# Kernel optimization log

Hardware: AMD Instinct MI355X
Metric: run time of the kernel (lower is better)

Reference implementation:

```python
import jax, jax.numpy as jnp
import numpy as np
import math

H_IMG, W_IMG = 800, 1216
STRIDES = [4, 8, 16, 32, 64]
SIZES = [32, 64, 128, 256, 512]
RATIOS = [0.5, 1.0, 2.0]
NUM_PER_LEVEL = [(-(-H_IMG // s)) * (-(-W_IMG // s)) * len(RATIOS) for s in STRIDES]
A_TOTAL = sum(NUM_PER_LEVEL)  # 728973
B = 4
PRE_NMS = 1000   # pre_nms_top_n['testing']
POST_NMS = 1000  # post_nms_top_n['testing']
NMS_TH = 0.7
MIN_SIZE = 1e-3
BBOX_XFORM_CLIP = math.log(1000.0 / 16)
NEG = -1e10
LEVELS_NP = np.repeat(np.arange(len(NUM_PER_LEVEL)), NUM_PER_LEVEL).astype(np.int32)


def _make_anchors():
    out = []
    for stride, size in zip(STRIDES, SIZES):
        fh, fw = -(-H_IMG // stride), -(-W_IMG // stride)
        r = np.sqrt(np.asarray(RATIOS, dtype=np.float64))
        ws, hs = size / r, size * r
        base = np.stack([-ws / 2, -hs / 2, ws / 2, hs / 2], axis=1)  # [3,4]
        sx = np.arange(fw, dtype=np.float64) * stride
        sy = np.arange(fh, dtype=np.float64) * stride
        gy, gx = np.meshgrid(sy, sx, indexing='ij')
        shifts = np.stack([gx.ravel(), gy.ravel(), gx.ravel(), gy.ravel()], axis=1)
        out.append((shifts[:, None, :] + base[None]).reshape(-1, 4))
    return np.concatenate(out, 0).astype(np.float32)


def setup_inputs() -> dict:
    key = jax.random.key(0)
    k1, k2 = jax.random.split(key)
    objectness = jax.random.normal(k1, (B, A_TOTAL), dtype=jnp.float32)
    deltas = jax.random.normal(k2, (B, A_TOTAL, 4), dtype=jnp.float32) * 0.2
    anchors = jnp.asarray(_make_anchors())
    return {'objectness': objectness, 'deltas': deltas, 'anchors': anchors}


def _decode(deltas, anchors):
    # BoxCoder.decode with weights (1,1,1,1)
    wa = anchors[:, 2] - anchors[:, 0]
    ha = anchors[:, 3] - anchors[:, 1]
    cxa = anchors[:, 0] + 0.5 * wa
    cya = anchors[:, 1] + 0.5 * ha
    dx, dy = deltas[..., 0], deltas[..., 1]
    dw = jnp.minimum(deltas[..., 2], BBOX_XFORM_CLIP)
    dh = jnp.minimum(deltas[..., 3], BBOX_XFORM_CLIP)
    cx = dx * wa + cxa
    cy = dy * ha + cya
    w = jnp.exp(dw) * wa
    h = jnp.exp(dh) * ha
    return jnp.stack([cx - 0.5 * w, cy - 0.5 * h, cx + 0.5 * w, cy + 0.5 * h], axis=-1)


def _topk_per_level(obj):
    # _get_top_n_idx: independent top-k within each anchor level, indices offset
    idxs, off = [], 0
    for n in NUM_PER_LEVEL:
        k = min(PRE_NMS, n)
        _, ti = jax.lax.top_k(obj[:, off:off + n], k)
        idxs.append(ti + off)
        off += n
    return jnp.concatenate(idxs, axis=1)


def _pairwise_iou(b):
    area = (b[:, 2] - b[:, 0]) * (b[:, 3] - b[:, 1])
    lt = jnp.maximum(b[:, None, :2], b[None, :, :2])
    rb = jnp.minimum(b[:, None, 2:], b[None, :, 2:])
    wh = jnp.clip(rb - lt, 0.0)
    inter = wh[..., 0] * wh[..., 1]
    return inter / (area[:, None] + area[None, :] - inter)


def _filter_image(boxes, scores, lvl):
    # clip_boxes_to_image
    x1 = jnp.clip(boxes[:, 0], 0.0, W_IMG)
    y1 = jnp.clip(boxes[:, 1], 0.0, H_IMG)
    x2 = jnp.clip(boxes[:, 2], 0.0, W_IMG)
    y2 = jnp.clip(boxes[:, 3], 0.0, H_IMG)
    boxes = jnp.stack([x1, y1, x2, y2], axis=1)
    # remove_small_boxes (as a validity mask; fixed shapes under jit)
    valid = ((x2 - x1) >= MIN_SIZE) & ((y2 - y1) >= MIN_SIZE)
    scores = jnp.where(valid, scores, NEG)
    N = boxes.shape[0]
    # batched_nms: offset boxes per level so levels never overlap
    sg_boxes = jax.lax.stop_gradient(boxes)
    offset = lvl.astype(boxes.dtype) * (sg_boxes.max() + 1.0)
    order = jnp.argsort(-jax.lax.stop_gradient(scores))
    iou = _pairwise_iou(sg_boxes[order] + offset[order][:, None])  # [N,N]
    idx = jnp.arange(N)
    def body(i, keep):
        sup = (iou[i] > NMS_TH) & keep[i] & (idx > i)
        return keep & ~sup
    keep = jax.lax.fori_loop(0, N, body, valid[order])
    # kept entries in score order, then truncate to POST_NMS (fixed shape)
    prio = jnp.where(keep, idx, N)
    sel = jnp.argsort(prio)[:POST_NMS]
    kept = keep[sel]
    src = order[sel]
    out_b = jnp.where(kept[:, None], boxes[src], 0.0)
    out_s = jnp.where(kept, scores[src], NEG)
    return out_b, out_s


def reference(objectness, deltas, anchors):
    proposals = _decode(deltas, anchors)                      # [B,A,4]
    top_idx = _topk_per_level(objectness)                     # [B,5000]
    obj_sel = jnp.take_along_axis(objectness, top_idx, axis=1)
    prop_sel = jnp.take_along_axis(proposals, top_idx[..., None], axis=1)
    lvl_sel = jnp.asarray(LEVELS_NP)[top_idx]
    boxes, scores = jax.vmap(_filter_image)(prop_sel, obj_sel, lvl_sel)
    return boxes, scores  # [B,POST_NMS,4], [B,POST_NMS]
```

## Files before the change

kernel.cpp:

```cpp
#include <hip/hip_runtime.h>
#include <stdint.h>

#pragma clang fp contract(off)

#define B_IMGS   4
#define NLVL     5
#define A_TOTAL  242991
#define NSEL     4741
#define NBUCK    8192
#define BSHIFT   19
#define CAND_CAP 2048
#define POST_NMS 1000
#define NBL      (B_IMGS * NLVL)
#define NMS_TH   0.7f
#define NEGV     (-1e10f)
#define W_IMGF   1216.0f
#define H_IMGF   800.0f
#define MIN_SZ   1e-3f
#define BBOX_CLIP 4.135166556742356f

__device__ __forceinline__ int lvl_k(int l) { return (l == 4) ? 741 : 1000; }

__device__ __forceinline__ unsigned flipf(float f) {
    unsigned u = __float_as_uint(f);
    return u ^ (unsigned)(((int)u >> 31) | 0x80000000);
}
__device__ __forceinline__ float unflipf(unsigned os) {
    unsigned u = (os & 0x80000000u) ? (os ^ 0x80000000u) : ~os;
    return __uint_as_float(u);
}

__device__ __forceinline__ void async_cp16(const void* g, void* l) {
    __builtin_amdgcn_global_load_lds(
        (const __attribute__((address_space(1))) unsigned*)g,
        (__attribute__((address_space(3))) unsigned*)l,
        16, 0, 0);
}

static constexpr size_t SZ_HIST    = (size_t)NBL * NBUCK * sizeof(unsigned);
static constexpr size_t OFF_CNT    = SZ_HIST;
static constexpr size_t OFF_BOXMAX = OFF_CNT + NBL * sizeof(unsigned);
static constexpr size_t ZERO_BYTES = OFF_BOXMAX + B_IMGS * sizeof(unsigned);
static constexpr size_t OFF_CAND   = (ZERO_BYTES + 15) & ~(size_t)15;
static constexpr size_t OFF_SEL    = OFF_CAND + (size_t)NBL * CAND_CAP * 8;
static constexpr size_t OFF_BOXR   = OFF_SEL + (size_t)B_IMGS * NSEL * 8;
static constexpr size_t OFF_SCR    = OFF_BOXR + (size_t)B_IMGS * NSEL * 16;
static constexpr size_t OFF_BOXL   = OFF_SCR + (size_t)B_IMGS * NSEL * 4;
static constexpr size_t OFF_VAL    = OFF_BOXL + (size_t)B_IMGS * NSEL * 16;
static constexpr size_t OFF_RMAP   = OFF_VAL + (size_t)B_IMGS * NSEL * 4;
static constexpr size_t OFF_KEEP   = OFF_RMAP + (size_t)B_IMGS * NSEL * 4;
static constexpr size_t OFF_MASK   = OFF_KEEP + (size_t)B_IMGS * NSEL * 4;
static constexpr size_t WS_NEED    = OFF_MASK + (size_t)NBL * 1024 * 16 * 8;

#define HBLK_PER_IMG 34
__global__ void k_hist(const float* __restrict__ obj, unsigned* __restrict__ hist) {
    __shared__ unsigned lh[NBUCK];
    const int tid = threadIdx.x;
    const int b = blockIdx.x / HBLK_PER_IMG;
    const int r = blockIdx.x - b * HBLK_PER_IMG;
    int l, sub, chunk, lstart, n;
    if (r < 24)      { l = 0; sub = r;      chunk = 7600; lstart = 0;      n = 182400; }
    else if (r < 30) { l = 1; sub = r - 24; chunk = 7600; lstart = 182400; n = 45600; }
    else if (r < 32) { l = 2; sub = r - 30; chunk = 5700; lstart = 228000; n = 11400; }
    else if (r == 32){ l = 3; sub = 0;      chunk = 2850; lstart = 239400; n = 2850; }
    else             { l = 4; sub = 0;      chunk = 741;  lstart = 242250; n = 741; }
    #pragma unroll
    for (int i = tid; i < NBUCK; i += 512) lh[i] = 0;
    __syncthreads();
    const int s0 = sub * chunk;
    const int cnt = min(chunk, n - s0);
    const float* src = obj + (size_t)b * A_TOTAL + lstart + s0;
    for (int i = tid; i < cnt; i += 512) {
        unsigned os = flipf(src[i]);
        atomicAdd(&lh[os >> BSHIFT], 1u);
    }
    __syncthreads();
    unsigned* gh = hist + (size_t)(b * NLVL + l) * NBUCK;
    for (int i = tid; i < NBUCK; i += 512) {
        unsigned v = lh[i];
        if (v) atomicAdd(&gh[i], v);
    }
}

#define CBLK_PER_IMG 65
__global__ void k_compact(const float* __restrict__ obj, const unsigned* __restrict__ hist,
                          unsigned* __restrict__ cnt, unsigned long long* __restrict__ cand) {
    __shared__ unsigned long long sbuf[CAND_CAP];
    __shared__ unsigned part[256];
    __shared__ unsigned wsum[4];
    __shared__ unsigned fcnt[4];
    __shared__ unsigned s_cum, s_thr, lcnt, gbase;
    const int tid = threadIdx.x;
    const int b = blockIdx.x / CBLK_PER_IMG;
    const int r = blockIdx.x - b * CBLK_PER_IMG;
    int l, sub, chunk, lstart, n;
    if (r < 48)      { l = 0; sub = r;      chunk = 3800; lstart = 0;      n = 182400; }
    else if (r < 60) { l = 1; sub = r - 48; chunk = 3800; lstart = 182400; n = 45600; }
    else if (r < 63) { l = 2; sub = r - 60; chunk = 3800; lstart = 228000; n = 11400; }
    else if (r == 63){ l = 3; sub = 0;      chunk = 2850; lstart = 239400; n = 2850; }
    else             { l = 4; sub = 0;      chunk = 741;  lstart = 242250; n = 741; }
    const int bl = b * NLVL + l;
    const int kl = lvl_k(l);
    const unsigned* h = hist + (size_t)bl * NBUCK;
    {
        unsigned s = 0;
        for (int i = 0; i < 32; ++i) s += h[tid * 32 + i];
        part[tid] = s;
    }
    if (tid == 0) { lcnt = 0; s_cum = 0; }
    __syncthreads();
    const int lane = tid & 63, wv = tid >> 6;
    unsigned x = part[255 - tid];
    #pragma unroll
    for (int d = 1; d < 64; d <<= 1) {
        unsigned up = __shfl_up(x, d);
        if (lane >= d) x += up;
    }
    if (lane == 63) wsum[wv] = x;
    __syncthreads();
    unsigned add = 0;
    #pragma unroll
    for (int u = 0; u < 3; ++u) if (u < wv) add += wsum[u];
    const unsigned suffix = x + add;
    unsigned long long bm = __ballot(suffix >= (unsigned)kl);
    if (lane == 0) fcnt[wv] = (unsigned)__popcll(bm);
    __syncthreads();
    const int chnk = (int)(fcnt[0] + fcnt[1] + fcnt[2] + fcnt[3]) - 1;
    if ((255 - tid) == chnk + 1) s_cum = suffix;
    __syncthreads();
    if (wv == 0) {
        unsigned y = (lane < 32) ? h[chnk * 32 + (31 - lane)] : 0u;
        #pragma unroll
        for (int d = 1; d < 32; d <<= 1) {
            unsigned up = __shfl_up(y, d);
            if (lane >= d) y += up;
        }
        unsigned suf2 = s_cum + y;
        unsigned long long bm2 = __ballot((lane < 32) && (suf2 >= (unsigned)kl));
        if (lane == 0) {
            int istar = (int)__popcll(bm2) - 1;
            s_thr = (unsigned)(chnk * 32 + istar);
        }
    }
    __syncthreads();
    const unsigned T = s_thr;
    const int s0 = sub * chunk;
    const int m = min(chunk, n - s0);
    const int abase = lstart + s0;
    const float* src = obj + (size_t)b * A_TOTAL + abase;
    for (int i = tid; i < m; i += 256) {
        unsigned os = flipf(src[i]);
        if ((os >> BSHIFT) >= T) {
            unsigned slot = atomicAdd(&lcnt, 1u);
            if (slot < CAND_CAP)
                sbuf[slot] = (((unsigned long long)(~os)) << 32) | (unsigned)(abase + i);
        }
    }
    __syncthreads();
    unsigned total = lcnt; if (total > CAND_CAP) total = CAND_CAP;
    if (tid == 0) gbase = atomicAdd(&cnt[bl], total);
    __syncthreads();
    const unsigned gb = gbase;
    for (unsigned i = tid; i < total; i += 256) {
        unsigned g = gb + i;
        if (g < CAND_CAP)
            cand[(size_t)bl * CAND_CAP + g] = sbuf[i];
    }
}

__global__ void k_sortlevel(const unsigned long long* __restrict__ cand,
                            const unsigned* __restrict__ cnt,
                            unsigned long long* __restrict__ sel) {
    __shared__ unsigned long long keys[CAND_CAP];
    const int bl = blockIdx.x;
    const int b = bl / NLVL, l = bl - (bl / NLVL) * NLVL;
    const int tid = threadIdx.x;
    int m = (int)cnt[bl];
    if (m > CAND_CAP) m = CAND_CAP;
    for (int i = tid; i < CAND_CAP; i += 1024)
        keys[i] = (i < m) ? cand[(size_t)bl * CAND_CAP + i] : ~0ULL;
    __syncthreads();
    for (int k = 2; k <= CAND_CAP; k <<= 1) {
        for (int j = k >> 1; j > 0; j >>= 1) {
            int i = ((tid / j) * (j << 1)) + (tid % j);
            int p = i + j;
            bool up = ((i & k) == 0);
            unsigned long long a = keys[i], c = keys[p];
            if ((a > c) == up) { keys[i] = c; keys[p] = a; }
            __syncthreads();
        }
    }
    int kl = lvl_k(l);
    for (int q = tid; q < kl; q += 1024)
        sel[(size_t)b * NSEL + l * 1000 + q] = keys[q];
}

__device__ __forceinline__ int lbound_lds(const unsigned long long* s, int len,
                                          unsigned long long key) {
    int lo = 0, hi = len;
    while (lo < hi) {
        int mid = (lo + hi) >> 1;
        if (s[mid] < key) lo = mid + 1; else hi = mid;
    }
    return lo;
}

__global__ void k_decode(const float* __restrict__ deltas, const float* __restrict__ anchors,
                         const unsigned long long* __restrict__ sel,
                         float* __restrict__ boxes_r, float* __restrict__ score_r,
                         float* __restrict__ boxes_l, int* __restrict__ valid_l,
                         int* __restrict__ rankmap, unsigned* __restrict__ boxmax) {
    __shared__ unsigned long long skey[NSEL];
    __shared__ float wmax[16];
    const int b = blockIdx.y;
    const int tid = threadIdx.x;
    for (int i = tid; i < NSEL; i += 1024)
        skey[i] = sel[(size_t)b * NSEL + i];
    __syncthreads();

    int p = blockIdx.x * 1024 + tid;
    bool on = p < NSEL;
    float mx = 0.0f;
    if (on) {
        int l = p / 1000;
        int q = p - l * 1000;
        unsigned long long key = skey[p];
        unsigned a = (unsigned)(key & 0xFFFFFFFFu);
        unsigned os = ~((unsigned)(key >> 32));
        if (a >= A_TOTAL) a = 0;
        float score = unflipf(os);
        int r = q;
        for (int l2 = 0; l2 < NLVL; ++l2) {
            if (l2 == l) continue;
            r += lbound_lds(skey + l2 * 1000, lvl_k(l2), key);
        }
        const float* dv = deltas + ((size_t)b * A_TOTAL + a) * 4;
        const float* av = anchors + (size_t)a * 4;
        float ax1 = av[0], ay1 = av[1], ax2 = av[2], ay2 = av[3];
        float wa = ax2 - ax1, ha = ay2 - ay1;
        float cxa = ax1 + 0.5f * wa, cya = ay1 + 0.5f * ha;
        float dx = dv[0], dy = dv[1];
        float dw = fminf(dv[2], BBOX_CLIP), dh = fminf(dv[3], BBOX_CLIP);
        float cx = dx * wa + cxa, cy = dy * ha + cya;
        float w = expf(dw) * wa, h = expf(dh) * ha;
        float x1 = cx - 0.5f * w, y1 = cy - 0.5f * h;
        float x2 = cx + 0.5f * w, y2 = cy + 0.5f * h;
        float x1c = fminf(fmaxf(x1, 0.0f), W_IMGF);
        float y1c = fminf(fmaxf(y1, 0.0f), H_IMGF);
        float x2c = fminf(fmaxf(x2, 0.0f), W_IMGF);
        float y2c = fminf(fmaxf(y2, 0.0f), H_IMGF);
        int valid = ((x2c - x1c) >= MIN_SZ) && ((y2c - y1c) >= MIN_SZ);
        mx = fmaxf(fmaxf(x1c, y1c), fmaxf(x2c, y2c));
        size_t rp = (size_t)b * NSEL + r;
        boxes_r[rp * 4 + 0] = x1c; boxes_r[rp * 4 + 1] = y1c;
        boxes_r[rp * 4 + 2] = x2c; boxes_r[rp * 4 + 3] = y2c;
        score_r[rp] = score;
        size_t pp = (size_t)b * NSEL + p;
        boxes_l[pp * 4 + 0] = x1c; boxes_l[pp * 4 + 1] = y1c;
        boxes_l[pp * 4 + 2] = x2c; boxes_l[pp * 4 + 3] = y2c;
        valid_l[pp] = valid;
        rankmap[pp] = r;
    }
    #pragma unroll
    for (int o = 32; o > 0; o >>= 1)
        mx = fmaxf(mx, __shfl_xor(mx, o));
    if ((tid & 63) == 0) wmax[tid >> 6] = mx;
    __syncthreads();
    if (tid == 0) {
        float m2 = wmax[0];
        #pragma unroll
        for (int i = 1; i < 16; ++i) m2 = fmaxf(m2, wmax[i]);
        atomicMax(boxmax + b, __float_as_uint(m2));
    }
}

__global__ void k_mask(const float* __restrict__ boxes_l, const unsigned* __restrict__ boxmax,
                       unsigned long long* __restrict__ mask) {
    int bl = blockIdx.z;
    int b = bl / NLVL, l = bl - b * NLVL;
    int kl = lvl_k(l);
    int w = blockIdx.x, rg = blockIdx.y, tid = threadIdx.x;
    if (rg * 256 >= kl) return;
    float M = __uint_as_float(boxmax[b]) + 1.0f;
    float off = (float)l * M;
    __shared__ float cb[64][5];
    int j0 = w * 64;
    if (tid < 64) {
        int j = j0 + tid;
        if (j < kl) {
            const float* bp = boxes_l + ((size_t)b * NSEL + l * 1000 + j) * 4;
            float x1 = bp[0] + off, y1 = bp[1] + off, x2 = bp[2] + off, y2 = bp[3] + off;
            cb[tid][0] = x1; cb[tid][1] = y1; cb[tid][2] = x2; cb[tid][3] = y2;
            cb[tid][4] = (x2 - x1) * (y2 - y1);
        }
    }
    __syncthreads();
    int i = rg * 256 + tid;
    if (i >= kl) return;
    unsigned long long word = 0;
    if (j0 + 63 > i) {
        const float* bp = boxes_l + ((size_t)b * NSEL + l * 1000 + i) * 4;
        float ix1 = bp[0] + off, iy1 = bp[1] + off, ix2 = bp[2] + off, iy2 = bp[3] + off;
        float ai = (ix2 - ix1) * (iy2 - iy1);
        int jmax = min(64, kl - j0);
        for (int bb = 0; bb < jmax; ++bb) {
            int jj = j0 + bb;
            if (jj <= i) continue;
            float ltx = fmaxf(ix1, cb[bb][0]), lty = fmaxf(iy1, cb[bb][1]);
            float rbx = fminf(ix2, cb[bb][2]), rby = fminf(iy2, cb[bb][3]);
            float ww = fmaxf(rbx - ltx, 0.0f), hh = fmaxf(rby - lty, 0.0f);
            float inter = ww * hh;
            float iou = inter / ((ai + cb[bb][4]) - inter);
            if (iou > NMS_TH) word |= (1ULL << bb);
        }
    }
    mask[((size_t)bl * 1024 + i) * 16 + w] = word;
}

__global__ void k_resolve(const int* __restrict__ valid_l, const int* __restrict__ rankmap,
                          const unsigned long long* __restrict__ mask, int* __restrict__ keep_r) {
    const int bl = blockIdx.x;
    const int b = bl / NLVL, l = bl - b * NLVL;
    const int kl = lvl_k(l);
    const int lane = threadIdx.x;
    __shared__ __align__(16) unsigned long long sbufA[64 * 16];
    __shared__ __align__(16) unsigned long long sbufB[64 * 16];
    const int base = b * NSEL + l * 1000;

    unsigned long long keep_w = 0;
    for (int c = 0; c < 16; ++c) {
        int q = c * 64 + lane;
        int vv = (q < kl) ? valid_l[base + q] : 0;
        unsigned long long bm = __ballot(vv);
        if (lane == c) keep_w = bm;
    }

    const int nch = (kl + 63) >> 6;
    const char* mbyte = (const char*)(mask + (size_t)bl * 1024 * 16);

    {
        const char* g0 = mbyte + (size_t)lane * 16;
        #pragma unroll
        for (int j = 0; j < 8; ++j)
            async_cp16(g0 + j * 1024, (char*)sbufA + j * 1024);
    }

    for (int c = 0; c < nch; ++c) {
        unsigned long long* cur = (c & 1) ? sbufB : sbufA;
        unsigned long long* nxt = (c & 1) ? sbufA : sbufB;
        __syncthreads();
        if (c + 1 < nch) {
            const char* g1 = mbyte + (size_t)(c + 1) * 8192 + (size_t)lane * 16;
            #pragma unroll
            for (int j = 0; j < 8; ++j)
                async_cp16(g1 + j * 1024, (char*)nxt + j * 1024);
        }
        unsigned long long kw = __shfl(keep_w, c);
        if (kw) {
            unsigned long long diag = cur[lane * 16 + c];
            unsigned dlo = (unsigned)diag, dhi = (unsigned)(diag >> 32);
            unsigned long long nz = __ballot(diag != 0ULL);
            unsigned long long rem = kw & nz;
            while (rem) {
                int r = __ffsll((long long)rem) - 1;
                unsigned lo = __builtin_amdgcn_readlane(dlo, r);
                unsigned hi = __builtin_amdgcn_readlane(dhi, r);
                unsigned long long d = ((unsigned long long)hi << 32) | lo;
                kw &= ~d;
                rem &= ~(d | (1ULL << r));
            }
            unsigned long long supp = 0;
            if (lane < 16) {
                #pragma unroll
                for (int r = 0; r < 64; ++r) {
                    unsigned long long m = cur[r * 16 + lane];
                    supp |= (((kw >> r) & 1ULL) ? m : 0ULL);
                }
            }
            if (lane == c) keep_w = kw;
            else if (lane < 16 && lane > c) keep_w &= ~supp;
        }
    }
    __syncthreads();
    for (int c = 0; c < 16; ++c) {
        unsigned long long kwc = __shfl(keep_w, c);
        int q = c * 64 + lane;
        if (q < kl)
            keep_r[b * NSEL + rankmap[base + q]] = (int)((kwc >> lane) & 1ULL);
    }
}

__global__ void k_output(const int* __restrict__ keep_r, const float* __restrict__ boxes_r,
                         const float* __restrict__ score_r, float* __restrict__ out) {
    int b = blockIdx.x, tid = threadIdx.x;
    float* ob = out + (size_t)b * POST_NMS * 4;
    float* osc = out + (size_t)B_IMGS * POST_NMS * 4 + (size_t)b * POST_NMS;
    for (int p = tid; p < POST_NMS; p += 1024) {
        ob[p * 4 + 0] = 0.0f; ob[p * 4 + 1] = 0.0f;
        ob[p * 4 + 2] = 0.0f; ob[p * 4 + 3] = 0.0f;
        osc[p] = NEGV;
    }
    __syncthreads();
    const int CH = 5;
    int base = tid * CH;
    int cnt = 0;
    #pragma unroll
    for (int k = 0; k < CH; ++k) {
        int r = base + k;
        if (r < NSEL) cnt += keep_r[b * NSEL + r];
    }
    __shared__ int ps[1024];
    ps[tid] = cnt;
    __syncthreads();
    for (int ofs = 1; ofs < 1024; ofs <<= 1) {
        int v = (tid >= ofs) ? ps[tid - ofs] : 0;
        __syncthreads();
        ps[tid] += v;
        __syncthreads();
    }
    int p = ps[tid] - cnt;
    #pragma unroll
    for (int k = 0; k < CH; ++k) {
        int r = base + k;
        if (r < NSEL && keep_r[b * NSEL + r]) {
            if (p < POST_NMS) {
                const float* bp = boxes_r + ((size_t)b * NSEL + r) * 4;
                ob[p * 4 + 0] = bp[0]; ob[p * 4 + 1] = bp[1];
                ob[p * 4 + 2] = bp[2]; ob[p * 4 + 3] = bp[3];
                osc[p] = score_r[(size_t)b * NSEL + r];
            }
            ++p;
        }
    }
}

extern "C" void kernel_launch(void* const* d_in, const int* in_sizes, int n_in,
                              void* d_out, int out_size, void* d_ws, size_t ws_size,
                              hipStream_t stream) {
    const float* obj     = (const float*)d_in[0];
    const float* deltas  = (const float*)d_in[1];
    const float* anchors = (const float*)d_in[2];
    float* out = (float*)d_out;

    char* ws = (char*)d_ws;
    unsigned*            hist    = (unsigned*)(ws);
    unsigned*            cnt     = (unsigned*)(ws + OFF_CNT);
    unsigned*            boxmax  = (unsigned*)(ws + OFF_BOXMAX);
    unsigned long long*  cand    = (unsigned long long*)(ws + OFF_CAND);
    unsigned long long*  sel     = (unsigned long long*)(ws + OFF_SEL);
    float*               boxes_r = (float*)(ws + OFF_BOXR);
    float*               score_r = (float*)(ws + OFF_SCR);
    float*               boxes_l = (float*)(ws + OFF_BOXL);
    int*                 valid_l = (int*)(ws + OFF_VAL);
    int*                 rankmap = (int*)(ws + OFF_RMAP);
    int*                 keep_r  = (int*)(ws + OFF_KEEP);
    unsigned long long*  maskp   = (unsigned long long*)(ws + OFF_MASK);

    (void)in_sizes; (void)n_in; (void)out_size; (void)ws_size; (void)WS_NEED;

    hipMemsetAsync(d_ws, 0, ZERO_BYTES, stream);

    k_hist<<<B_IMGS * HBLK_PER_IMG, 512, 0, stream>>>(obj, hist);
    k_compact<<<B_IMGS * CBLK_PER_IMG, 256, 0, stream>>>(obj, hist, cnt, cand);
    k_sortlevel<<<NBL, 1024, 0, stream>>>(cand, cnt, sel);
    k_decode<<<dim3(5, B_IMGS), 1024, 0, stream>>>(
        deltas, anchors, sel, boxes_r, score_r, boxes_l, valid_l, rankmap, boxmax);
    k_mask<<<dim3(16, 4, NBL), 256, 0, stream>>>(boxes_l, boxmax, maskp);
    k_resolve<<<NBL, 64, 0, stream>>>(valid_l, rankmap, maskp, keep_r);
    k_output<<<B_IMGS, 1024, 0, stream>>>(keep_r, boxes_r, score_r, out);
}
```

Before: 183.3 us.

## Fuse histogram, compaction and level sort into one per-level top-k kernel

The separate histogram, compaction and per-level bitonic sort kernels are replaced by a single kernel with one 1024-thread block per (image, level). That block builds the histogram in LDS, finds the threshold bucket, compacts candidates and sorts them without global intermediates. The global box max becomes per-block writes that the mask kernel reduces itself, so no atomics are needed and the workspace memset goes away. This removes several launches and global round trips, but the largest level is now scanned twice by a single block, which limits parallelism and may lengthen the critical path.

Result: slower. 251.5 us (+37.2%).

```diff
diff --git a/kernel.cpp b/kernel.cpp
--- a/kernel.cpp
+++ b/kernel.cpp
@@ -20,6 +20,15 @@
 #define BBOX_CLIP 4.135166556742356f
 
 __device__ __forceinline__ int lvl_k(int l) { return (l == 4) ? 741 : 1000; }
+__device__ __forceinline__ void lvl_span(int l, int& lstart, int& n) {
+    switch (l) {
+    case 0: lstart = 0;      n = 182400; break;
+    case 1: lstart = 182400; n = 45600;  break;
+    case 2: lstart = 228000; n = 11400;  break;
+    case 3: lstart = 239400; n = 2850;   break;
+    default:lstart = 242250; n = 741;    break;
+    }
+}
 
 __device__ __forceinline__ unsigned flipf(float f) {
     unsigned u = __float_as_uint(f);
@@ -37,162 +46,117 @@
         16, 0, 0);
 }
 
-static constexpr size_t SZ_HIST    = (size_t)NBL * NBUCK * sizeof(unsigned);
-static constexpr size_t OFF_CNT    = SZ_HIST;
-static constexpr size_t OFF_BOXMAX = OFF_CNT + NBL * sizeof(unsigned);
-static constexpr size_t ZERO_BYTES = OFF_BOXMAX + B_IMGS * sizeof(unsigned);
-static constexpr size_t OFF_CAND   = (ZERO_BYTES + 15) & ~(size_t)15;
-static constexpr size_t OFF_SEL    = OFF_CAND + (size_t)NBL * CAND_CAP * 8;
-static constexpr size_t OFF_BOXR   = OFF_SEL + (size_t)B_IMGS * NSEL * 8;
-static constexpr size_t OFF_SCR    = OFF_BOXR + (size_t)B_IMGS * NSEL * 16;
-static constexpr size_t OFF_BOXL   = OFF_SCR + (size_t)B_IMGS * NSEL * 4;
-static constexpr size_t OFF_VAL    = OFF_BOXL + (size_t)B_IMGS * NSEL * 16;
-static constexpr size_t OFF_RMAP   = OFF_VAL + (size_t)B_IMGS * NSEL * 4;
-static constexpr size_t OFF_KEEP   = OFF_RMAP + (size_t)B_IMGS * NSEL * 4;
-static constexpr size_t OFF_MASK   = OFF_KEEP + (size_t)B_IMGS * NSEL * 4;
-static constexpr size_t WS_NEED    = OFF_MASK + (size_t)NBL * 1024 * 16 * 8;
-
-#define HBLK_PER_IMG 34
-__global__ void k_hist(const float* __restrict__ obj, unsigned* __restrict__ hist) {
+static constexpr size_t OFF_BM5   = 0;
+static constexpr size_t OFF_SEL   = 128;
+static constexpr size_t OFF_BOXR  = OFF_SEL  + (size_t)B_IMGS * NSEL * 8;
+static constexpr size_t OFF_SCR   = OFF_BOXR + (size_t)B_IMGS * NSEL * 16;
+static constexpr size_t OFF_BOXL  = OFF_SCR  + (size_t)B_IMGS * NSEL * 4;
+static constexpr size_t OFF_VAL   = OFF_BOXL + (size_t)B_IMGS * NSEL * 16;
+static constexpr size_t OFF_RMAP  = OFF_VAL  + (size_t)B_IMGS * NSEL * 4;
+static constexpr size_t OFF_KEEP  = OFF_RMAP + (size_t)B_IMGS * NSEL * 4;
+static constexpr size_t OFF_MASK  = (OFF_KEEP + (size_t)B_IMGS * NSEL * 4 + 15) & ~(size_t)15;
+static constexpr size_t WS_NEED   = OFF_MASK + (size_t)NBL * 1024 * 16 * 8;
+
+__global__ __launch_bounds__(1024) void k_topk(const float* __restrict__ obj,
+                                               unsigned long long* __restrict__ sel) {
     __shared__ unsigned lh[NBUCK];
-    const int tid = threadIdx.x;
-    const int b = blockIdx.x / HBLK_PER_IMG;
-    const int r = blockIdx.x - b * HBLK_PER_IMG;
-    int l, sub, chunk, lstart, n;
-    if (r < 24)      { l = 0; sub = r;      chunk = 7600; lstart = 0;      n = 182400; }
-    else if (r < 30) { l = 1; sub = r - 24; chunk = 7600; lstart = 182400; n = 45600; }
-    else if (r < 32) { l = 2; sub = r - 30; chunk = 5700; lstart = 228000; n = 11400; }
-    else if (r == 32){ l = 3; sub = 0;      chunk = 2850; lstart = 239400; n = 2850; }
-    else             { l = 4; sub = 0;      chunk = 741;  lstart = 242250; n = 741; }
-    #pragma unroll
-    for (int i = tid; i < NBUCK; i += 512) lh[i] = 0;
-    __syncthreads();
-    const int s0 = sub * chunk;
-    const int cnt = min(chunk, n - s0);
-    const float* src = obj + (size_t)b * A_TOTAL + lstart + s0;
-    for (int i = tid; i < cnt; i += 512) {
-        unsigned os = flipf(src[i]);
-        atomicAdd(&lh[os >> BSHIFT], 1u);
-    }
-    __syncthreads();
-    unsigned* gh = hist + (size_t)(b * NLVL + l) * NBUCK;
-    for (int i = tid; i < NBUCK; i += 512) {
-        unsigned v = lh[i];
-        if (v) atomicAdd(&gh[i], v);
-    }
-}
-
-#define CBLK_PER_IMG 65
-__global__ void k_compact(const float* __restrict__ obj, const unsigned* __restrict__ hist,
-                          unsigned* __restrict__ cnt, unsigned long long* __restrict__ cand) {
-    __shared__ unsigned long long sbuf[CAND_CAP];
+    __shared__ unsigned long long sbf[CAND_CAP];
     __shared__ unsigned part[256];
     __shared__ unsigned wsum[4];
     __shared__ unsigned fcnt[4];
-    __shared__ unsigned s_cum, s_thr, lcnt, gbase;
+    __shared__ unsigned s_cum, s_thr, lcnt;
     const int tid = threadIdx.x;
-    const int b = blockIdx.x / CBLK_PER_IMG;
-    const int r = blockIdx.x - b * CBLK_PER_IMG;
-    int l, sub, chunk, lstart, n;
-    if (r < 48)      { l = 0; sub = r;      chunk = 3800; lstart = 0;      n = 182400; }
-    else if (r < 60) { l = 1; sub = r - 48; chunk = 3800; lstart = 182400; n = 45600; }
-    else if (r < 63) { l = 2; sub = r - 60; chunk = 3800; lstart = 228000; n = 11400; }
-    else if (r == 63){ l = 3; sub = 0;      chunk = 2850; lstart = 239400; n = 2850; }
-    else             { l = 4; sub = 0;      chunk = 741;  lstart = 242250; n = 741; }
-    const int bl = b * NLVL + l;
+    const int bl = blockIdx.x;
+    const int b = bl / NLVL, l = bl - (bl / NLVL) * NLVL;
+    int lstart, n;
+    lvl_span(l, lstart, n);
     const int kl = lvl_k(l);
-    const unsigned* h = hist + (size_t)bl * NBUCK;
-    {
+
+    for (int i = tid; i < NBUCK; i += 1024) lh[i] = 0;
+    if (tid == 0) { lcnt = 0; s_cum = 0; }
+    __syncthreads();
+
+    const float* src = obj + (size_t)b * A_TOTAL + lstart;
+    for (int i = tid; i < n; i += 1024)
+        atomicAdd(&lh[flipf(src[i]) >> BSHIFT], 1u);
+    __syncthreads();
+
+    if (tid < 256) {
         unsigned s = 0;
-        for (int i = 0; i < 32; ++i) s += h[tid * 32 + i];
+        #pragma unroll
+        for (int i = 0; i < 32; ++i) s += lh[tid * 32 + ((i + tid) & 31)];
         part[tid] = s;
     }
-    if (tid == 0) { lcnt = 0; s_cum = 0; }
-    __syncthreads();
+    __syncthreads();
+
     const int lane = tid & 63, wv = tid >> 6;
-    unsigned x = part[255 - tid];
-    #pragma unroll
-    for (int d = 1; d < 64; d <<= 1) {
-        unsigned up = __shfl_up(x, d);
-        if (lane >= d) x += up;
-    }
-    if (lane == 63) wsum[wv] = x;
-    __syncthreads();
-    unsigned add = 0;
-    #pragma unroll
-    for (int u = 0; u < 3; ++u) if (u < wv) add += wsum[u];
-    const unsigned suffix = x + add;
-    unsigned long long bm = __ballot(suffix >= (unsigned)kl);
-    if (lane == 0) fcnt[wv] = (unsigned)__popcll(bm);
+    unsigned suffix = 0;
+    if (tid < 256) {
+        unsigned x = part[255 - tid];
+        #pragma unroll
+        for (int d = 1; d < 64; d <<= 1) {
+            unsigned up = __shfl_up(x, d);
+            if (lane >= d) x += up;
+        }
+        if (lane == 63) wsum[wv] = x;
+        suffix = x;
+    }
+    __syncthreads();
+    if (tid < 256) {
+        unsigned add = 0;
+        #pragma unroll
+        for (int u = 0; u < 3; ++u) if (u < wv) add += wsum[u];
+        suffix += add;
+        unsigned long long bm = __ballot(suffix >= (unsigned)kl);
+        if (lane == 0) fcnt[wv] = (unsigned)__popcll(bm);
+    }
     __syncthreads();
     const int chnk = (int)(fcnt[0] + fcnt[1] + fcnt[2] + fcnt[3]) - 1;
-    if ((255 - tid) == chnk + 1) s_cum = suffix;
-    __syncthreads();
-    if (wv == 0) {
-        unsigned y = (lane < 32) ? h[chnk * 32 + (31 - lane)] : 0u;
+    if (tid < 256 && (255 - tid) == chnk + 1) s_cum = suffix;
+    __syncthreads();
+    if (tid < 64) {
+        unsigned y = (tid < 32) ? lh[chnk * 32 + (31 - tid)] : 0u;
         #pragma unroll
         for (int d = 1; d < 32; d <<= 1) {
             unsigned up = __shfl_up(y, d);
-            if (lane >= d) y += up;
+            if (tid >= d) y += up;
         }
         unsigned suf2 = s_cum + y;
-        unsigned long long bm2 = __ballot((lane < 32) && (suf2 >= (unsigned)kl));
-        if (lane == 0) {
+        unsigned long long bm2 = __ballot((tid < 32) && (suf2 >= (unsigned)kl));
+        if (tid == 0) {
             int istar = (int)__popcll(bm2) - 1;
             s_thr = (unsigned)(chnk * 32 + istar);
         }
     }
     __syncthreads();
     const unsigned T = s_thr;
-    const int s0 = sub * chunk;
-    const int m = min(chunk, n - s0);
-    const int abase = lstart + s0;
-    const float* src = obj + (size_t)b * A_TOTAL + abase;
-    for (int i = tid; i < m; i += 256) {
+
+    for (int i = tid; i < n; i += 1024) {
         unsigned os = flipf(src[i]);
         if ((os >> BSHIFT) >= T) {
             unsigned slot = atomicAdd(&lcnt, 1u);
             if (slot < CAND_CAP)
-                sbuf[slot] = (((unsigned long long)(~os)) << 32) | (unsigned)(abase + i);
-        }
-    }
-    __syncthreads();
-    unsigned total = lcnt; if (total > CAND_CAP) total = CAND_CAP;
-    if (tid == 0) gbase = atomicAdd(&cnt[bl], total);
-    __syncthreads();
-    const unsigned gb = gbase;
-    for (unsigned i = tid; i < total; i += 256) {
-        unsigned g = gb + i;
-        if (g < CAND_CAP)
-            cand[(size_t)bl * CAND_CAP + g] = sbuf[i];
-    }
-}
-
-__global__ void k_sortlevel(const unsigned long long* __restrict__ cand,
-                            const unsigned* __restrict__ cnt,
-                            unsigned long long* __restrict__ sel) {
-    __shared__ unsigned long long keys[CAND_CAP];
-    const int bl = blockIdx.x;
-    const int b = bl / NLVL, l = bl - (bl / NLVL) * NLVL;
-    const int tid = threadIdx.x;
-    int m = (int)cnt[bl];
-    if (m > CAND_CAP) m = CAND_CAP;
+                sbf[slot] = (((unsigned long long)(~os)) << 32) | (unsigned)(lstart + i);
+        }
+    }
+    __syncthreads();
+    unsigned m = lcnt; if (m > CAND_CAP) m = CAND_CAP;
     for (int i = tid; i < CAND_CAP; i += 1024)
-        keys[i] = (i < m) ? cand[(size_t)bl * CAND_CAP + i] : ~0ULL;
-    __syncthreads();
+        if ((unsigned)i >= m) sbf[i] = ~0ULL;
+    __syncthreads();
+
     for (int k = 2; k <= CAND_CAP; k <<= 1) {
         for (int j = k >> 1; j > 0; j >>= 1) {
             int i = ((tid / j) * (j << 1)) + (tid % j);
             int p = i + j;
             bool up = ((i & k) == 0);
-            unsigned long long a = keys[i], c = keys[p];
-            if ((a > c) == up) { keys[i] = c; keys[p] = a; }
+            unsigned long long a = sbf[i], c = sbf[p];
+            if ((a > c) == up) { sbf[i] = c; sbf[p] = a; }
             __syncthreads();
         }
     }
-    int kl = lvl_k(l);
     for (int q = tid; q < kl; q += 1024)
-        sel[(size_t)b * NSEL + l * 1000 + q] = keys[q];
+        sel[(size_t)b * NSEL + l * 1000 + q] = sbf[q];
 }
 
 __device__ __forceinline__ int lbound_lds(const unsigned long long* s, int len,
@@ -209,7 +173,7 @@
                          const unsigned long long* __restrict__ sel,
                          float* __restrict__ boxes_r, float* __restrict__ score_r,
                          float* __restrict__ boxes_l, int* __restrict__ valid_l,
-                         int* __restrict__ rankmap, unsigned* __restrict__ boxmax) {
+                         int* __restrict__ rankmap, unsigned* __restrict__ boxmax5) {
     __shared__ unsigned long long skey[NSEL];
     __shared__ float wmax[16];
     const int b = blockIdx.y;
@@ -270,18 +234,21 @@
         float m2 = wmax[0];
         #pragma unroll
         for (int i = 1; i < 16; ++i) m2 = fmaxf(m2, wmax[i]);
-        atomicMax(boxmax + b, __float_as_uint(m2));
-    }
-}
-
-__global__ void k_mask(const float* __restrict__ boxes_l, const unsigned* __restrict__ boxmax,
+        boxmax5[b * 5 + blockIdx.x] = __float_as_uint(m2);
+    }
+}
+
+__global__ void k_mask(const float* __restrict__ boxes_l, const unsigned* __restrict__ boxmax5,
                        unsigned long long* __restrict__ mask) {
     int bl = blockIdx.z;
     int b = bl / NLVL, l = bl - b * NLVL;
     int kl = lvl_k(l);
     int w = blockIdx.x, rg = blockIdx.y, tid = threadIdx.x;
     if (rg * 256 >= kl) return;
-    float M = __uint_as_float(boxmax[b]) + 1.0f;
+    float M = __uint_as_float(boxmax5[b * 5 + 0]);
+    #pragma unroll
+    for (int j = 1; j < 5; ++j) M = fmaxf(M, __uint_as_float(boxmax5[b * 5 + j]));
+    M += 1.0f;
     float off = (float)l * M;
     __shared__ float cb[64][5];
     int j0 = w * 64;
@@ -443,10 +410,7 @@
     float* out = (float*)d_out;
 
     char* ws = (char*)d_ws;
-    unsigned*            hist    = (unsigned*)(ws);
-    unsigned*            cnt     = (unsigned*)(ws + OFF_CNT);
-    unsigned*            boxmax  = (unsigned*)(ws + OFF_BOXMAX);
-    unsigned long long*  cand    = (unsigned long long*)(ws + OFF_CAND);
+    unsigned*            boxmax5 = (unsigned*)(ws + OFF_BM5);
     unsigned long long*  sel     = (unsigned long long*)(ws + OFF_SEL);
     float*               boxes_r = (float*)(ws + OFF_BOXR);
     float*               score_r = (float*)(ws + OFF_SCR);
@@ -458,14 +422,10 @@
 
     (void)in_sizes; (void)n_in; (void)out_size; (void)ws_size; (void)WS_NEED;
 
-    hipMemsetAsync(d_ws, 0, ZERO_BYTES, stream);
-
-    k_hist<<<B_IMGS * HBLK_PER_IMG, 512, 0, stream>>>(obj, hist);
-    k_compact<<<B_IMGS * CBLK_PER_IMG, 256, 0, stream>>>(obj, hist, cnt, cand);
-    k_sortlevel<<<NBL, 1024, 0, stream>>>(cand, cnt, sel);
+    k_topk<<<NBL, 1024, 0, stream>>>(obj, sel);
     k_decode<<<dim3(5, B_IMGS), 1024, 0, stream>>>(
-        deltas, anchors, sel, boxes_r, score_r, boxes_l, valid_l, rankmap, boxmax);
-    k_mask<<<dim3(16, 4, NBL), 256, 0, stream>>>(boxes_l, boxmax, maskp);
+        deltas, anchors, sel, boxes_r, score_r, boxes_l, valid_l, rankmap, boxmax5);
+    k_mask<<<dim3(16, 4, NBL), 256, 0, stream>>>(boxes_l, boxmax5, maskp);
     k_resolve<<<NBL, 64, 0, stream>>>(valid_l, rankmap, maskp, keep_r);
     k_output<<<B_IMGS, 1024, 0, stream>>>(keep_r, boxes_r, score_r, out);
 }
```
